# Performance work log

Measured on AMD Instinct MI355X. Metric: run time of the kernel, lower is better.

The kernel has to match this reference:

```python
import jax, jax.numpy as jnp
import numpy as np
import math

K = 8
MOMENTUM = 0.999


def _gelu(x):
    c = math.sqrt(2.0 / math.pi)
    return 0.5 * x * (1.0 + jnp.tanh(c * (x + 0.044715 * x ** 3)))


def _normalize(v, eps=1e-12):
    n = jnp.linalg.norm(v, axis=-1, keepdims=True)
    return v / jnp.maximum(n, eps)


def setup_inputs() -> dict:
    key = jax.random.key(0)
    k1, k2 = jax.random.split(key)
    B, T, D = 4, 4096, 2048
    x = jax.random.normal(k1, (B, T, D), dtype=jnp.float32)
    prototypes = _normalize(jax.random.normal(k2, (K, D), dtype=jnp.float32))
    log_tau = jnp.asarray(math.log(2.0), dtype=jnp.float32)
    log_blend = jnp.asarray(math.log(0.3 / 0.7), dtype=jnp.float32)
    return {"x": x, "prototypes": prototypes, "log_tau": log_tau, "log_blend": log_blend}


def reference(x, prototypes, log_tau, log_blend):
    tau = jnp.exp(log_tau)
    alpha = jax.nn.sigmoid(log_blend)
    B, T, D = x.shape
    x_flat = jax.lax.stop_gradient(x.reshape(-1, D))  # [N, D], detached

    P_norm = _normalize(prototypes)                  # [K, D]
    xn = _normalize(x_flat, eps=1e-8)                # [N, D]

    sims = jnp.clip(xn @ P_norm.T, -1.0, 1.0)        # [N, K]
    assignments = jnp.argmax(sims, axis=-1)          # [N]

    # masked per-cluster mean via segment-sum (vectorized over K)
    sums = jax.ops.segment_sum(x_flat, assignments, num_segments=K)       # [K, D]
    counts = jax.ops.segment_sum(jnp.ones((x_flat.shape[0],), x.dtype),
                                 assignments, num_segments=K)             # [K]
    has = (counts > 0)[:, None]
    centroids = jnp.where(has, sums / jnp.maximum(counts, 1.0)[:, None], prototypes)
    new_P = _normalize(centroids)

    P2 = MOMENTUM * prototypes + (1.0 - MOMENTUM) * new_P
    P2n = _normalize(P2, eps=1e-8)

    sims2 = jnp.clip(xn @ P2n.T, -1.0, 1.0)          # [N, K]
    dists = jnp.clip(1.0 - jnp.max(sims2, axis=-1), 0.0, 2.0)
    novelty = (1.0 - jnp.exp(-tau * dists)).reshape(B, T)

    scale = jnp.clip(1.0 - alpha + alpha * novelty[..., None], 0.1, 10.0)
    return _gelu(x * scale)
```

## Files before the change

kernel.cpp:

```cpp
#include <hip/hip_runtime.h>

#define DDIM  2048
#define KC    8
#define NCH   32
#define TPB_A 16
#define TPB_C 16

typedef float nfloat4 __attribute__((ext_vector_type(4)));
typedef unsigned short ushortv8 __attribute__((ext_vector_type(8)));
typedef unsigned short ushortv4 __attribute__((ext_vector_type(4)));

__device__ __forceinline__ void nt_store4(const float4& v, float* p){
  nfloat4 nv; nv.x = v.x; nv.y = v.y; nv.z = v.z; nv.w = v.w;
  __builtin_nontemporal_store(nv, (nfloat4*)p);
}

__device__ __forceinline__ unsigned short f2bf(float f){
  unsigned u = __float_as_uint(f);
  u += 0x7fffu + ((u >> 16) & 1u);
  return (unsigned short)(u >> 16);
}
__device__ __forceinline__ float bf2f(unsigned short h){
  return __uint_as_float(((unsigned)h) << 16);
}
__device__ __forceinline__ float bflo(unsigned u){ return __uint_as_float(u << 16); }
__device__ __forceinline__ float bfhi(unsigned u){ return __uint_as_float(u & 0xffff0000u); }

__device__ __forceinline__ float wave_sum(float v){
  #pragma unroll
  for (int off = 32; off > 0; off >>= 1)
    v += __shfl_xor(v, off, 64);
  return v;
}

__device__ __forceinline__ float butterfly8(float v[8], int t){
  {
    const bool h = (t & 1);
    #pragma unroll
    for (int j = 0; j < 4; ++j){
      float s    = h ? v[j]   : v[j+4];
      float keep = h ? v[j+4] : v[j];
      v[j] = keep + __shfl_xor(s, 1, 64);
    }
  }
  {
    const bool h = (t & 2);
    #pragma unroll
    for (int j = 0; j < 2; ++j){
      float s    = h ? v[j]   : v[j+2];
      float keep = h ? v[j+2] : v[j];
      v[j] = keep + __shfl_xor(s, 2, 64);
    }
  }
  {
    const bool h = (t & 4);
    float s    = h ? v[0] : v[1];
    float keep = h ? v[1] : v[0];
    v[0] = keep + __shfl_xor(s, 4, 64);
  }
  v[0] += __shfl_xor(v[0], 8, 64);
  v[0] += __shfl_xor(v[0], 16, 64);
  v[0] += __shfl_xor(v[0], 32, 64);
  return v[0];
}

__device__ __forceinline__ float gelu_tanh(float v){
  const float c = 0.7978845608028654f;
  float tt = c * v * (1.0f + 0.044715f * v * v);
  float e  = __expf(2.0f * tt);
  float th = 1.0f - 2.0f / (e + 1.0f);
  return 0.5f * v * (1.0f + th);
}

__global__ __launch_bounds__(256)
void k_pre(const float* __restrict__ proto, unsigned short* __restrict__ pbf)
{
  const int k = blockIdx.x, t = threadIdx.x;
  const int wave = t >> 6, lane = t & 63;
  __shared__ float sred[4];
  const int d0 = 4*t, d1 = 1024 + 4*t;
  float4 a = *(const float4*)(proto + k*DDIM + d0);
  float4 b = *(const float4*)(proto + k*DDIM + d1);
  float ss = a.x*a.x + a.y*a.y + a.z*a.z + a.w*a.w
           + b.x*b.x + b.y*b.y + b.z*b.z + b.w*b.w;
  ss = wave_sum(ss);
  if (lane == 0) sred[wave] = ss;
  __syncthreads();
  ss = sred[0] + sred[1] + sred[2] + sred[3];
  const float inv = 1.0f / fmaxf(sqrtf(ss), 1e-12f);
  ushortv4 o0, o1;
  o0[0]=f2bf(a.x*inv); o0[1]=f2bf(a.y*inv); o0[2]=f2bf(a.z*inv); o0[3]=f2bf(a.w*inv);
  o1[0]=f2bf(b.x*inv); o1[1]=f2bf(b.y*inv); o1[2]=f2bf(b.z*inv); o1[3]=f2bf(b.w*inv);
  *(ushortv4*)(pbf + k*DDIM + d0) = o0;
  *(ushortv4*)(pbf + k*DDIM + d1) = o1;
}

__global__ __launch_bounds__(256, 4)
void k_assign(const float* __restrict__ x, const unsigned short* __restrict__ pbf,
              unsigned short* __restrict__ part, float* __restrict__ pcnts, int ntok)
{
  __shared__ unsigned short Pl[KC*DDIM];
  __shared__ int asg[TPB_A];

  const int t = threadIdx.x;
  const int wave = t >> 6, lane = t & 63;

  #pragma unroll
  for (int j = 0; j < 8; ++j){
    const int e = (j*256 + t)*8;
    *(ushortv8*)(Pl + e) = *(const ushortv8*)(pbf + e);
  }
  __syncthreads();

  const int tok_base = blockIdx.x * TPB_A;

  {
    const int tl0 = wave*4;
    float4 X[8], N[8];
    int tok = tok_base + tl0;
    if (tok < ntok){
      #pragma unroll
      for (int j = 0; j < 8; ++j)
        X[j] = *(const float4*)(x + (size_t)tok*DDIM + j*256 + 4*lane);
    }
    #pragma unroll
    for (int i = 0; i < 4; ++i){
      const int tok_i = tok_base + tl0 + i;
      const bool ldn = (i < 3) && (tok_i + 1 < ntok);
      if (ldn){
        #pragma unroll
        for (int j = 0; j < 8; ++j)
          N[j] = *(const float4*)(x + (size_t)(tok_i+1)*DDIM + j*256 + 4*lane);
      }
      if (tok_i < ntok){
        float v[KC];
        #pragma unroll
        for (int k = 0; k < KC; ++k){
          float s = 0.f;
          #pragma unroll
          for (int j = 0; j < 8; ++j){
            uint2 u = *(const uint2*)((const unsigned*)Pl + k*1024 + j*128 + 2*lane);
            s += X[j].x*bflo(u.x) + X[j].y*bfhi(u.x)
               + X[j].z*bflo(u.y) + X[j].w*bfhi(u.y);
          }
          v[k] = s;
        }
        float bv = butterfly8(v, lane);
        int   bi = ((lane&1)<<2) | (lane&2) | ((lane>>2)&1);
        #pragma unroll
        for (int off = 1; off < 8; off <<= 1){
          float ov = __shfl_xor(bv, off, 64);
          int   oi = __shfl_xor(bi, off, 64);
          if (ov > bv || (ov == bv && oi < bi)){ bv = ov; bi = oi; }
        }
        if (lane == 0) asg[tl0 + i] = bi;
      }
      if (ldn){
        #pragma unroll
        for (int j = 0; j < 8; ++j) X[j] = N[j];
      }
    }
  }
  __syncthreads();

  const int d0 = 4*t, d1 = 1024 + 4*t;
  float4 acc0[KC], acc1[KC];
  float cnt[KC];
  #pragma unroll
  for (int k = 0; k < KC; ++k){
    acc0[k] = make_float4(0.f,0.f,0.f,0.f);
    acc1[k] = make_float4(0.f,0.f,0.f,0.f);
    cnt[k] = 0.f;
  }
  #pragma unroll
  for (int i = 0; i < TPB_A; ++i){
    const int tok = tok_base + i;
    if (tok < ntok){
      const int a = __builtin_amdgcn_readfirstlane(asg[i]);
      float4 xa = *(const float4*)(x + (size_t)tok*DDIM + d0);
      float4 xb = *(const float4*)(x + (size_t)tok*DDIM + d1);
      #pragma unroll
      for (int k = 0; k < KC; ++k){
        if (a == k){
          acc0[k].x += xa.x; acc0[k].y += xa.y; acc0[k].z += xa.z; acc0[k].w += xa.w;
          acc1[k].x += xb.x; acc1[k].y += xb.y; acc1[k].z += xb.z; acc1[k].w += xb.w;
          cnt[k] += 1.f;
        }
      }
    }
  }
  unsigned short* dst = part + (size_t)blockIdx.x * (KC*DDIM);
  #pragma unroll
  for (int k = 0; k < KC; ++k){
    ushortv4 o0, o1;
    o0[0]=f2bf(acc0[k].x); o0[1]=f2bf(acc0[k].y); o0[2]=f2bf(acc0[k].z); o0[3]=f2bf(acc0[k].w);
    o1[0]=f2bf(acc1[k].x); o1[1]=f2bf(acc1[k].y); o1[2]=f2bf(acc1[k].z); o1[3]=f2bf(acc1[k].w);
    *(ushortv4*)(dst + k*DDIM + d0) = o0;
    *(ushortv4*)(dst + k*DDIM + d1) = o1;
  }
  if (t == 0){
    #pragma unroll
    for (int k = 0; k < KC; ++k) pcnts[blockIdx.x*KC + k] = cnt[k];
  }
}

__global__ __launch_bounds__(256)
void k_reduce1(const unsigned short* __restrict__ part, const float* __restrict__ pcnts,
               float* __restrict__ stage2, float* __restrict__ cnt2, int nbA, int cs)
{
  const int ch = blockIdx.x >> 3;
  const int g  = blockIdx.x & 7;
  const int t  = threadIdx.x;
  const int col = g*2048 + t*8;
  const int b0 = ch*cs;

  float acc[8] = {0.f,0.f,0.f,0.f,0.f,0.f,0.f,0.f};
  for (int i = 0; i < cs; ++i){
    const int b = b0 + i;
    if (b < nbA){
      ushortv8 v = *(const ushortv8*)(part + (size_t)b*(KC*DDIM) + col);
      #pragma unroll
      for (int j = 0; j < 8; ++j) acc[j] += bf2f(v[j]);
    }
  }
  float4 o0 = make_float4(acc[0],acc[1],acc[2],acc[3]);
  float4 o1 = make_float4(acc[4],acc[5],acc[6],acc[7]);
  *(float4*)(stage2 + (size_t)ch*(KC*DDIM) + col)     = o0;
  *(float4*)(stage2 + (size_t)ch*(KC*DDIM) + col + 4) = o1;

  if (g == 0 && t < KC){
    float c = 0.f;
    for (int i = 0; i < cs; ++i){
      const int b = b0 + i;
      if (b < nbA) c += pcnts[b*KC + t];
    }
    cnt2[ch*KC + t] = c;
  }
}

__global__ __launch_bounds__(256)
void k_mid(const float* __restrict__ stage2, const float* __restrict__ cnt2,
           const float* __restrict__ proto, unsigned short* __restrict__ p2nbf)
{
  const int k = blockIdx.x, t = threadIdx.x;
  const int wave = t >> 6, lane = t & 63;
  __shared__ float s1[4], s2[4];
  const int d0 = 4*t, d1 = 1024 + 4*t;

  float4 a = make_float4(0.f,0.f,0.f,0.f), b = make_float4(0.f,0.f,0.f,0.f);
  #pragma unroll
  for (int ch = 0; ch < NCH; ++ch){
    const float* p = stage2 + (size_t)ch*(KC*DDIM) + k*DDIM;
    float4 u = *(const float4*)(p + d0);
    float4 w = *(const float4*)(p + d1);
    a.x += u.x; a.y += u.y; a.z += u.z; a.w += u.w;
    b.x += w.x; b.y += w.y; b.z += w.z; b.w += w.w;
  }
  float c = 0.f;
  #pragma unroll
  for (int ch = 0; ch < NCH; ++ch) c += cnt2[ch*KC + k];

  float4 pr0 = *(const float4*)(proto + k*DDIM + d0);
  float4 pr1 = *(const float4*)(proto + k*DDIM + d1);

  float4 c0, c1;
  if (c > 0.f){
    const float inv = 1.0f / fmaxf(c, 1.0f);
    c0.x=a.x*inv; c0.y=a.y*inv; c0.z=a.z*inv; c0.w=a.w*inv;
    c1.x=b.x*inv; c1.y=b.y*inv; c1.z=b.z*inv; c1.w=b.w*inv;
  } else { c0 = pr0; c1 = pr1; }

  float ss = c0.x*c0.x + c0.y*c0.y + c0.z*c0.z + c0.w*c0.w
           + c1.x*c1.x + c1.y*c1.y + c1.z*c1.z + c1.w*c1.w;
  ss = wave_sum(ss);
  if (lane == 0) s1[wave] = ss;
  __syncthreads();
  ss = s1[0] + s1[1] + s1[2] + s1[3];
  const float invc = 1.0f / fmaxf(sqrtf(ss), 1e-12f);

  const float m = 0.999f, om = 1.0f - 0.999f;
  float4 p20, p21;
  p20.x = m*pr0.x + om*c0.x*invc; p20.y = m*pr0.y + om*c0.y*invc;
  p20.z = m*pr0.z + om*c0.z*invc; p20.w = m*pr0.w + om*c0.w*invc;
  p21.x = m*pr1.x + om*c1.x*invc; p21.y = m*pr1.y + om*c1.y*invc;
  p21.z = m*pr1.z + om*c1.z*invc; p21.w = m*pr1.w + om*c1.w*invc;

  float ss2 = p20.x*p20.x + p20.y*p20.y + p20.z*p20.z + p20.w*p20.w
            + p21.x*p21.x + p21.y*p21.y + p21.z*p21.z + p21.w*p21.w;
  ss2 = wave_sum(ss2);
  if (lane == 0) s2[wave] = ss2;
  __syncthreads();
  ss2 = s2[0] + s2[1] + s2[2] + s2[3];
  const float inv2 = 1.0f / fmaxf(sqrtf(ss2), 1e-8f);

  ushortv4 o0, o1;
  o0[0]=f2bf(p20.x*inv2); o0[1]=f2bf(p20.y*inv2); o0[2]=f2bf(p20.z*inv2); o0[3]=f2bf(p20.w*inv2);
  o1[0]=f2bf(p21.x*inv2); o1[1]=f2bf(p21.y*inv2); o1[2]=f2bf(p21.z*inv2); o1[3]=f2bf(p21.w*inv2);
  *(ushortv4*)(p2nbf + k*DDIM + d0) = o0;
  *(ushortv4*)(p2nbf + k*DDIM + d1) = o1;
}

__global__ __launch_bounds__(256, 4)
void k_final(const float* __restrict__ x, const unsigned short* __restrict__ p2nbf,
             const float* __restrict__ plt, const float* __restrict__ plb,
             float* __restrict__ out, int ntok)
{
  __shared__ unsigned short Pl[KC*DDIM];
  const int t = threadIdx.x;
  const int wave = t >> 6, lane = t & 63;

  #pragma unroll
  for (int j = 0; j < 8; ++j){
    const int e = (j*256 + t)*8;
    *(ushortv8*)(Pl + e) = *(const ushortv8*)(p2nbf + e);
  }
  __syncthreads();

  const float tau   = __expf(plt[0]);
  const float alpha = 1.0f / (1.0f + __expf(-plb[0]));

  const int tl0 = wave*4;
  const int tok_base = blockIdx.x * TPB_C;
  float4 X[8], N[8];
  {
    const int tok = tok_base + tl0;
    if (tok < ntok){
      #pragma unroll
      for (int j = 0; j < 8; ++j)
        X[j] = *(const float4*)(x + (size_t)tok*DDIM + j*256 + 4*lane);
    }
  }
  #pragma unroll
  for (int i = 0; i < 4; ++i){
    const int tok_i = tok_base + tl0 + i;
    const bool ldn = (i < 3) && (tok_i + 1 < ntok);
    if (ldn){
      #pragma unroll
      for (int j = 0; j < 8; ++j)
        N[j] = *(const float4*)(x + (size_t)(tok_i+1)*DDIM + j*256 + 4*lane);
    }
    if (tok_i < ntok){
      float ss = 0.f;
      #pragma unroll
      for (int j = 0; j < 8; ++j)
        ss += X[j].x*X[j].x + X[j].y*X[j].y + X[j].z*X[j].z + X[j].w*X[j].w;
      ss = wave_sum(ss);

      float v[KC];
      #pragma unroll
      for (int k = 0; k < KC; ++k){
        float s = 0.f;
        #pragma unroll
        for (int j = 0; j < 8; ++j){
          uint2 u = *(const uint2*)((const unsigned*)Pl + k*1024 + j*128 + 2*lane);
          s += X[j].x*bflo(u.x) + X[j].y*bfhi(u.x)
             + X[j].z*bflo(u.y) + X[j].w*bfhi(u.y);
        }
        v[k] = s;
      }
      float mx = butterfly8(v, lane);
      mx = fmaxf(mx, __shfl_xor(mx, 1, 64));
      mx = fmaxf(mx, __shfl_xor(mx, 2, 64));
      mx = fmaxf(mx, __shfl_xor(mx, 4, 64));

      const float inv  = 1.0f / fmaxf(sqrtf(ss), 1e-8f);
      const float s    = fminf(fmaxf(mx * inv, -1.0f), 1.0f);
      const float dist = fminf(fmaxf(1.0f - s, 0.0f), 2.0f);
      const float nov  = 1.0f - __expf(-tau * dist);
      float sc = 1.0f - alpha + alpha * nov;
      sc = fminf(fmaxf(sc, 0.1f), 10.0f);

      float* o = out + (size_t)tok_i*DDIM;
      #pragma unroll
      for (int j = 0; j < 8; ++j){
        float4 g;
        g.x = gelu_tanh(X[j].x*sc); g.y = gelu_tanh(X[j].y*sc);
        g.z = gelu_tanh(X[j].z*sc); g.w = gelu_tanh(X[j].w*sc);
        nt_store4(g, o + j*256 + 4*lane);
      }
    }
    if (ldn){
      #pragma unroll
      for (int j = 0; j < 8; ++j) X[j] = N[j];
    }
  }
}

extern "C" void kernel_launch(void* const* d_in, const int* in_sizes, int n_in,
                              void* d_out, int out_size, void* d_ws, size_t ws_size,
                              hipStream_t stream)
{
  const float* x         = (const float*)d_in[0];
  const float* proto     = (const float*)d_in[1];
  const float* log_tau   = (const float*)d_in[2];
  const float* log_blend = (const float*)d_in[3];
  float* out = (float*)d_out;
  float* ws  = (float*)d_ws;

  const int ntok = in_sizes[0] / DDIM;

  unsigned short* pbf    = (unsigned short*)(ws);
  unsigned short* p2nbf  = (unsigned short*)(ws + 8192);
  float*          pcnts  = ws + 16384;
  float*          cnt2   = ws + 24576;
  float*          stage2 = ws + 24832;
  unsigned short* part   = (unsigned short*)(ws + 549120);

  const int nbA = (ntok + TPB_A - 1) / TPB_A;
  const int nbC = (ntok + TPB_C - 1) / TPB_C;
  const int cs  = (nbA + NCH - 1) / NCH;

  k_pre    <<<KC,     256, 0, stream>>>(proto, pbf);
  k_assign <<<nbA,    256, 0, stream>>>(x, pbf, part, pcnts, ntok);
  k_reduce1<<<NCH*8,  256, 0, stream>>>(part, pcnts, stage2, cnt2, nbA, cs);
  k_mid    <<<KC,     256, 0, stream>>>(stage2, cnt2, proto, p2nbf);
  k_final  <<<nbC,    256, 0, stream>>>(x, p2nbf, log_tau, log_blend, out, ntok);
}
```

Baseline: 306.4 us.

## Fuse prototype normalization into assign, double tokens per block, single-pass reduce

Removes the separate prototype-normalization kernel by having every assign block normalize the prototypes into shared memory. Tokens per block are doubled in both assign and final, which halves the number of partial-sum slabs. The two-stage chunked reduction is replaced by one reduce kernel that sums across all blocks for each (cluster, column slice), and partial-sum traffic now uses nontemporal stores and loads. In exchange, each assign block repeats the prototype norm work, and there is less block-level parallelism. The counts reduction assumes nbA is at most 512.

```diff
diff --git a/kernel.cpp b/kernel.cpp
--- a/kernel.cpp
+++ b/kernel.cpp
@@ -2,9 +2,8 @@
 
 #define DDIM  2048
 #define KC    8
-#define NCH   32
-#define TPB_A 16
-#define TPB_C 16
+#define TPB_A 32
+#define TPB_C 32
 
 typedef float nfloat4 __attribute__((ext_vector_type(4)));
 typedef unsigned short ushortv8 __attribute__((ext_vector_type(8)));
@@ -13,6 +12,12 @@
 __device__ __forceinline__ void nt_store4(const float4& v, float* p){
   nfloat4 nv; nv.x = v.x; nv.y = v.y; nv.z = v.z; nv.w = v.w;
   __builtin_nontemporal_store(nv, (nfloat4*)p);
+}
+__device__ __forceinline__ void nt_store_us4(const ushortv4& v, unsigned short* p){
+  __builtin_nontemporal_store(v, (ushortv4*)p);
+}
+__device__ __forceinline__ ushortv8 nt_load_us8(const unsigned short* p){
+  return __builtin_nontemporal_load((const ushortv8*)p);
 }
 
 __device__ __forceinline__ unsigned short f2bf(float f){
@@ -72,61 +77,68 @@
   return 0.5f * v * (1.0f + th);
 }
 
-__global__ __launch_bounds__(256)
-void k_pre(const float* __restrict__ proto, unsigned short* __restrict__ pbf)
-{
-  const int k = blockIdx.x, t = threadIdx.x;
-  const int wave = t >> 6, lane = t & 63;
-  __shared__ float sred[4];
-  const int d0 = 4*t, d1 = 1024 + 4*t;
-  float4 a = *(const float4*)(proto + k*DDIM + d0);
-  float4 b = *(const float4*)(proto + k*DDIM + d1);
-  float ss = a.x*a.x + a.y*a.y + a.z*a.z + a.w*a.w
-           + b.x*b.x + b.y*b.y + b.z*b.z + b.w*b.w;
-  ss = wave_sum(ss);
-  if (lane == 0) sred[wave] = ss;
-  __syncthreads();
-  ss = sred[0] + sred[1] + sred[2] + sred[3];
-  const float inv = 1.0f / fmaxf(sqrtf(ss), 1e-12f);
-  ushortv4 o0, o1;
-  o0[0]=f2bf(a.x*inv); o0[1]=f2bf(a.y*inv); o0[2]=f2bf(a.z*inv); o0[3]=f2bf(a.w*inv);
-  o1[0]=f2bf(b.x*inv); o1[1]=f2bf(b.y*inv); o1[2]=f2bf(b.z*inv); o1[3]=f2bf(b.w*inv);
-  *(ushortv4*)(pbf + k*DDIM + d0) = o0;
-  *(ushortv4*)(pbf + k*DDIM + d1) = o1;
-}
-
 __global__ __launch_bounds__(256, 4)
-void k_assign(const float* __restrict__ x, const unsigned short* __restrict__ pbf,
+void k_assign(const float* __restrict__ x, const float* __restrict__ proto,
               unsigned short* __restrict__ part, float* __restrict__ pcnts, int ntok)
 {
   __shared__ unsigned short Pl[KC*DDIM];
-  __shared__ int asg[TPB_A];
+  __shared__ float rednorm[4*KC];
+  __shared__ float sInv[KC];
+  __shared__ int   asg[TPB_A];
 
   const int t = threadIdx.x;
   const int wave = t >> 6, lane = t & 63;
-
-  #pragma unroll
-  for (int j = 0; j < 8; ++j){
-    const int e = (j*256 + t)*8;
-    *(ushortv8*)(Pl + e) = *(const ushortv8*)(pbf + e);
+  const int d0 = 4*t, d1 = 1024 + 4*t;
+
+  {
+    float4 Q0[KC], Q1[KC];
+    #pragma unroll
+    for (int k = 0; k < KC; ++k){
+      Q0[k] = *(const float4*)(proto + k*DDIM + d0);
+      Q1[k] = *(const float4*)(proto + k*DDIM + d1);
+    }
+    #pragma unroll
+    for (int k = 0; k < KC; ++k){
+      float ss = Q0[k].x*Q0[k].x + Q0[k].y*Q0[k].y + Q0[k].z*Q0[k].z + Q0[k].w*Q0[k].w
+               + Q1[k].x*Q1[k].x + Q1[k].y*Q1[k].y + Q1[k].z*Q1[k].z + Q1[k].w*Q1[k].w;
+      ss = wave_sum(ss);
+      if (lane == 0) rednorm[wave*KC + k] = ss;
+    }
+    __syncthreads();
+    if (t < KC){
+      float ss = rednorm[t] + rednorm[KC+t] + rednorm[2*KC+t] + rednorm[3*KC+t];
+      sInv[t] = 1.0f / fmaxf(sqrtf(ss), 1e-12f);
+    }
+    __syncthreads();
+    #pragma unroll
+    for (int k = 0; k < KC; ++k){
+      const float inv = sInv[k];
+      ushortv4 o0, o1;
+      o0[0]=f2bf(Q0[k].x*inv); o0[1]=f2bf(Q0[k].y*inv); o0[2]=f2bf(Q0[k].z*inv); o0[3]=f2bf(Q0[k].w*inv);
+      o1[0]=f2bf(Q1[k].x*inv); o1[1]=f2bf(Q1[k].y*inv); o1[2]=f2bf(Q1[k].z*inv); o1[3]=f2bf(Q1[k].w*inv);
+      *(ushortv4*)(Pl + k*DDIM + d0) = o0;
+      *(ushortv4*)(Pl + k*DDIM + d1) = o1;
+    }
   }
   __syncthreads();
 
   const int tok_base = blockIdx.x * TPB_A;
 
   {
-    const int tl0 = wave*4;
+    const int tl0 = wave*8;
     float4 X[8], N[8];
-    int tok = tok_base + tl0;
-    if (tok < ntok){
-      #pragma unroll
-      for (int j = 0; j < 8; ++j)
-        X[j] = *(const float4*)(x + (size_t)tok*DDIM + j*256 + 4*lane);
-    }
-    #pragma unroll
-    for (int i = 0; i < 4; ++i){
+    {
+      const int tok = tok_base + tl0;
+      if (tok < ntok){
+        #pragma unroll
+        for (int j = 0; j < 8; ++j)
+          X[j] = *(const float4*)(x + (size_t)tok*DDIM + j*256 + 4*lane);
+      }
+    }
+    #pragma unroll
+    for (int i = 0; i < 8; ++i){
       const int tok_i = tok_base + tl0 + i;
-      const bool ldn = (i < 3) && (tok_i + 1 < ntok);
+      const bool ldn = (i < 7) && (tok_i + 1 < ntok);
       if (ldn){
         #pragma unroll
         for (int j = 0; j < 8; ++j)
@@ -163,7 +175,6 @@
   }
   __syncthreads();
 
-  const int d0 = 4*t, d1 = 1024 + 4*t;
   float4 acc0[KC], acc1[KC];
   float cnt[KC];
   #pragma unroll
@@ -195,8 +206,8 @@
     ushortv4 o0, o1;
     o0[0]=f2bf(acc0[k].x); o0[1]=f2bf(acc0[k].y); o0[2]=f2bf(acc0[k].z); o0[3]=f2bf(acc0[k].w);
     o1[0]=f2bf(acc1[k].x); o1[1]=f2bf(acc1[k].y); o1[2]=f2bf(acc1[k].z); o1[3]=f2bf(acc1[k].w);
-    *(ushortv4*)(dst + k*DDIM + d0) = o0;
-    *(ushortv4*)(dst + k*DDIM + d1) = o1;
+    nt_store_us4(o0, dst + k*DDIM + d0);
+    nt_store_us4(o1, dst + k*DDIM + d1);
   }
   if (t == 0){
     #pragma unroll
@@ -205,41 +216,50 @@
 }
 
 __global__ __launch_bounds__(256)
-void k_reduce1(const unsigned short* __restrict__ part, const float* __restrict__ pcnts,
-               float* __restrict__ stage2, float* __restrict__ cnt2, int nbA, int cs)
+void k_reduce(const unsigned short* __restrict__ part, const float* __restrict__ pcnts,
+              float* __restrict__ csum, float* __restrict__ ccnt, int nbA)
 {
-  const int ch = blockIdx.x >> 3;
-  const int g  = blockIdx.x & 7;
-  const int t  = threadIdx.x;
-  const int col = g*2048 + t*8;
-  const int b0 = ch*cs;
-
-  float acc[8] = {0.f,0.f,0.f,0.f,0.f,0.f,0.f,0.f};
-  for (int i = 0; i < cs; ++i){
-    const int b = b0 + i;
-    if (b < nbA){
-      ushortv8 v = *(const ushortv8*)(part + (size_t)b*(KC*DDIM) + col);
-      #pragma unroll
-      for (int j = 0; j < 8; ++j) acc[j] += bf2f(v[j]);
-    }
-  }
-  float4 o0 = make_float4(acc[0],acc[1],acc[2],acc[3]);
-  float4 o1 = make_float4(acc[4],acc[5],acc[6],acc[7]);
-  *(float4*)(stage2 + (size_t)ch*(KC*DDIM) + col)     = o0;
-  *(float4*)(stage2 + (size_t)ch*(KC*DDIM) + col + 4) = o1;
-
-  if (g == 0 && t < KC){
-    float c = 0.f;
-    for (int i = 0; i < cs; ++i){
-      const int b = b0 + i;
-      if (b < nbA) c += pcnts[b*KC + t];
-    }
-    cnt2[ch*KC + t] = c;
-  }
+  const int k = blockIdx.x >> 4;
+  const int s = blockIdx.x & 15;
+  const int t = threadIdx.x;
+  const int slot = t & 15;
+  const int grp  = t >> 4;
+
+  __shared__ float cmb[16][16][8];
+  __shared__ float credn[4];
+
+  const size_t ebase = (size_t)k*DDIM + s*128 + slot*8;
+  float a[8] = {0.f,0.f,0.f,0.f,0.f,0.f,0.f,0.f};
+  for (int b = grp; b < nbA; b += 16){
+    ushortv8 v = nt_load_us8(part + (size_t)b*(KC*DDIM) + ebase);
+    #pragma unroll
+    for (int j = 0; j < 8; ++j) a[j] += bf2f(v[j]);
+  }
+  #pragma unroll
+  for (int j = 0; j < 8; ++j) cmb[grp][slot][j] = a[j];
+
+  float c = 0.f;
+  if (s == 0){
+    if (t < nbA)        c += pcnts[t*KC + k];
+    if (t + 256 < nbA)  c += pcnts[(t+256)*KC + k];
+    c = wave_sum(c);
+    if ((t & 63) == 0) credn[t >> 6] = c;
+  }
+  __syncthreads();
+
+  if (t < 128){
+    const int slot2 = t >> 3, j = t & 7;
+    float sum = 0.f;
+    #pragma unroll
+    for (int g = 0; g < 16; ++g) sum += cmb[g][slot2][j];
+    csum[(size_t)k*DDIM + s*128 + slot2*8 + j] = sum;
+  }
+  if (s == 0 && t == 0)
+    ccnt[k] = credn[0] + credn[1] + credn[2] + credn[3];
 }
 
 __global__ __launch_bounds__(256)
-void k_mid(const float* __restrict__ stage2, const float* __restrict__ cnt2,
+void k_mid(const float* __restrict__ csum, const float* __restrict__ ccnt,
            const float* __restrict__ proto, unsigned short* __restrict__ p2nbf)
 {
   const int k = blockIdx.x, t = threadIdx.x;
@@ -247,18 +267,9 @@
   __shared__ float s1[4], s2[4];
   const int d0 = 4*t, d1 = 1024 + 4*t;
 
-  float4 a = make_float4(0.f,0.f,0.f,0.f), b = make_float4(0.f,0.f,0.f,0.f);
-  #pragma unroll
-  for (int ch = 0; ch < NCH; ++ch){
-    const float* p = stage2 + (size_t)ch*(KC*DDIM) + k*DDIM;
-    float4 u = *(const float4*)(p + d0);
-    float4 w = *(const float4*)(p + d1);
-    a.x += u.x; a.y += u.y; a.z += u.z; a.w += u.w;
-    b.x += w.x; b.y += w.y; b.z += w.z; b.w += w.w;
-  }
-  float c = 0.f;
-  #pragma unroll
-  for (int ch = 0; ch < NCH; ++ch) c += cnt2[ch*KC + k];
+  float4 a = *(const float4*)(csum + k*DDIM + d0);
+  float4 b = *(const float4*)(csum + k*DDIM + d1);
+  const float c = ccnt[k];
 
   float4 pr0 = *(const float4*)(proto + k*DDIM + d0);
   float4 pr1 = *(const float4*)(proto + k*DDIM + d1);
@@ -319,7 +330,7 @@
   const float tau   = __expf(plt[0]);
   const float alpha = 1.0f / (1.0f + __expf(-plb[0]));
 
-  const int tl0 = wave*4;
+  const int tl0 = wave*8;
   const int tok_base = blockIdx.x * TPB_C;
   float4 X[8], N[8];
   {
@@ -331,9 +342,9 @@
     }
   }
   #pragma unroll
-  for (int i = 0; i < 4; ++i){
+  for (int i = 0; i < 8; ++i){
     const int tok_i = tok_base + tl0 + i;
-    const bool ldn = (i < 3) && (tok_i + 1 < ntok);
+    const bool ldn = (i < 7) && (tok_i + 1 < ntok);
     if (ldn){
       #pragma unroll
       for (int j = 0; j < 8; ++j)
@@ -399,20 +410,17 @@
 
   const int ntok = in_sizes[0] / DDIM;
 
-  unsigned short* pbf    = (unsigned short*)(ws);
-  unsigned short* p2nbf  = (unsigned short*)(ws + 8192);
-  float*          pcnts  = ws + 16384;
-  float*          cnt2   = ws + 24576;
-  float*          stage2 = ws + 24832;
-  unsigned short* part   = (unsigned short*)(ws + 549120);
+  unsigned short* p2nbf = (unsigned short*)(ws);
+  float*          pcnts = ws + 8192;
+  float*          csum  = ws + 12288;
+  float*          ccnt  = ws + 28672;
+  unsigned short* part  = (unsigned short*)(ws + 28688);
 
   const int nbA = (ntok + TPB_A - 1) / TPB_A;
   const int nbC = (ntok + TPB_C - 1) / TPB_C;
-  const int cs  = (nbA + NCH - 1) / NCH;
-
-  k_pre    <<<KC,     256, 0, stream>>>(proto, pbf);
-  k_assign <<<nbA,    256, 0, stream>>>(x, pbf, part, pcnts, ntok);
-  k_reduce1<<<NCH*8,  256, 0, stream>>>(part, pcnts, stage2, cnt2, nbA, cs);
-  k_mid    <<<KC,     256, 0, stream>>>(stage2, cnt2, proto, p2nbf);
-  k_final  <<<nbC,    256, 0, stream>>>(x, p2nbf, log_tau, log_blend, out, ntok);
-}
+
+  k_assign<<<nbA, 256, 0, stream>>>(x, proto, part, pcnts, ntok);
+  k_reduce<<<128, 256, 0, stream>>>(part, pcnts, csum, ccnt, nbA);
+  k_mid   <<<KC,  256, 0, stream>>>(csum, ccnt, proto, p2nbf);
+  k_final <<<nbC, 256, 0, stream>>>(x, p2nbf, log_tau, log_blend, out, ntok);
+}
```

After: 333.4 us. +8.8%, slower.

## Replace two-level chunked partial reduction with single-pass per-cluster column reduce

Applied to the files above, without the earlier changes.

The two-stage reduction (chunked partials into a stage2 buffer, then summed again in k_mid) is replaced by one k_reduce kernel. Each block owns a 64-element column strip of one cluster, strides over all partial blocks with 32 thread groups, and combines them in shared memory, so the stage2 buffer and k_mid's 32-way re-summation go away. The partial writes and reads now use nontemporal stores and loads to avoid polluting the cache. The readfirstlane on the assignment index is also dropped, which could make the branch non-uniform to the compiler and add scalar-to-vector overhead in k_assign.

```diff
diff --git a/kernel.cpp b/kernel.cpp
--- a/kernel.cpp
+++ b/kernel.cpp
@@ -2,7 +2,6 @@
 
 #define DDIM  2048
 #define KC    8
-#define NCH   32
 #define TPB_A 16
 #define TPB_C 16
 
@@ -13,6 +12,12 @@
 __device__ __forceinline__ void nt_store4(const float4& v, float* p){
   nfloat4 nv; nv.x = v.x; nv.y = v.y; nv.z = v.z; nv.w = v.w;
   __builtin_nontemporal_store(nv, (nfloat4*)p);
+}
+__device__ __forceinline__ void nt_store_us4(const ushortv4& v, unsigned short* p){
+  __builtin_nontemporal_store(v, (ushortv4*)p);
+}
+__device__ __forceinline__ ushortv8 nt_load_us8(const unsigned short* p){
+  return __builtin_nontemporal_load((const ushortv8*)p);
 }
 
 __device__ __forceinline__ unsigned short f2bf(float f){
@@ -176,7 +181,7 @@
   for (int i = 0; i < TPB_A; ++i){
     const int tok = tok_base + i;
     if (tok < ntok){
-      const int a = __builtin_amdgcn_readfirstlane(asg[i]);
+      const int a = asg[i];
       float4 xa = *(const float4*)(x + (size_t)tok*DDIM + d0);
       float4 xb = *(const float4*)(x + (size_t)tok*DDIM + d1);
       #pragma unroll
@@ -195,8 +200,8 @@
     ushortv4 o0, o1;
     o0[0]=f2bf(acc0[k].x); o0[1]=f2bf(acc0[k].y); o0[2]=f2bf(acc0[k].z); o0[3]=f2bf(acc0[k].w);
     o1[0]=f2bf(acc1[k].x); o1[1]=f2bf(acc1[k].y); o1[2]=f2bf(acc1[k].z); o1[3]=f2bf(acc1[k].w);
-    *(ushortv4*)(dst + k*DDIM + d0) = o0;
-    *(ushortv4*)(dst + k*DDIM + d1) = o1;
+    nt_store_us4(o0, dst + k*DDIM + d0);
+    nt_store_us4(o1, dst + k*DDIM + d1);
   }
   if (t == 0){
     #pragma unroll
@@ -205,41 +210,49 @@
 }
 
 __global__ __launch_bounds__(256)
-void k_reduce1(const unsigned short* __restrict__ part, const float* __restrict__ pcnts,
-               float* __restrict__ stage2, float* __restrict__ cnt2, int nbA, int cs)
-{
-  const int ch = blockIdx.x >> 3;
-  const int g  = blockIdx.x & 7;
-  const int t  = threadIdx.x;
-  const int col = g*2048 + t*8;
-  const int b0 = ch*cs;
-
-  float acc[8] = {0.f,0.f,0.f,0.f,0.f,0.f,0.f,0.f};
-  for (int i = 0; i < cs; ++i){
-    const int b = b0 + i;
-    if (b < nbA){
-      ushortv8 v = *(const ushortv8*)(part + (size_t)b*(KC*DDIM) + col);
-      #pragma unroll
-      for (int j = 0; j < 8; ++j) acc[j] += bf2f(v[j]);
-    }
-  }
-  float4 o0 = make_float4(acc[0],acc[1],acc[2],acc[3]);
-  float4 o1 = make_float4(acc[4],acc[5],acc[6],acc[7]);
-  *(float4*)(stage2 + (size_t)ch*(KC*DDIM) + col)     = o0;
-  *(float4*)(stage2 + (size_t)ch*(KC*DDIM) + col + 4) = o1;
-
-  if (g == 0 && t < KC){
-    float c = 0.f;
-    for (int i = 0; i < cs; ++i){
-      const int b = b0 + i;
-      if (b < nbA) c += pcnts[b*KC + t];
-    }
-    cnt2[ch*KC + t] = c;
-  }
+void k_reduce(const unsigned short* __restrict__ part, const float* __restrict__ pcnts,
+              float* __restrict__ csum, float* __restrict__ ccnt, int nbA)
+{
+  const int k = blockIdx.x >> 5;
+  const int s = blockIdx.x & 31;
+  const int t = threadIdx.x;
+  const int slot = t & 7;
+  const int grp  = t >> 3;
+
+  __shared__ float cmb[32][8][8];
+  __shared__ float credn[4];
+
+  const size_t ebase = (size_t)k*DDIM + s*64 + slot*8;
+  float a[8] = {0.f,0.f,0.f,0.f,0.f,0.f,0.f,0.f};
+  for (int b = grp; b < nbA; b += 32){
+    ushortv8 v = nt_load_us8(part + (size_t)b*(KC*DDIM) + ebase);
+    #pragma unroll
+    for (int j = 0; j < 8; ++j) a[j] += bf2f(v[j]);
+  }
+  #pragma unroll
+  for (int j = 0; j < 8; ++j) cmb[grp][slot][j] = a[j];
+
+  float c = 0.f;
+  if (s == 0){
+    for (int b = t; b < nbA; b += 256) c += pcnts[b*KC + k];
+    c = wave_sum(c);
+    if ((t & 63) == 0) credn[t >> 6] = c;
+  }
+  __syncthreads();
+
+  if (t < 64){
+    const int slot2 = t >> 3, j = t & 7;
+    float sum = 0.f;
+    #pragma unroll
+    for (int g = 0; g < 32; ++g) sum += cmb[g][slot2][j];
+    csum[(size_t)k*DDIM + s*64 + slot2*8 + j] = sum;
+  }
+  if (s == 0 && t == 0)
+    ccnt[k] = credn[0] + credn[1] + credn[2] + credn[3];
 }
 
 __global__ __launch_bounds__(256)
-void k_mid(const float* __restrict__ stage2, const float* __restrict__ cnt2,
+void k_mid(const float* __restrict__ csum, const float* __restrict__ ccnt,
            const float* __restrict__ proto, unsigned short* __restrict__ p2nbf)
 {
   const int k = blockIdx.x, t = threadIdx.x;
@@ -247,18 +260,9 @@
   __shared__ float s1[4], s2[4];
   const int d0 = 4*t, d1 = 1024 + 4*t;
 
-  float4 a = make_float4(0.f,0.f,0.f,0.f), b = make_float4(0.f,0.f,0.f,0.f);
-  #pragma unroll
-  for (int ch = 0; ch < NCH; ++ch){
-    const float* p = stage2 + (size_t)ch*(KC*DDIM) + k*DDIM;
-    float4 u = *(const float4*)(p + d0);
-    float4 w = *(const float4*)(p + d1);
-    a.x += u.x; a.y += u.y; a.z += u.z; a.w += u.w;
-    b.x += w.x; b.y += w.y; b.z += w.z; b.w += w.w;
-  }
-  float c = 0.f;
-  #pragma unroll
-  for (int ch = 0; ch < NCH; ++ch) c += cnt2[ch*KC + k];
+  float4 a = *(const float4*)(csum + k*DDIM + d0);
+  float4 b = *(const float4*)(csum + k*DDIM + d1);
+  const float c = ccnt[k];
 
   float4 pr0 = *(const float4*)(proto + k*DDIM + d0);
   float4 pr1 = *(const float4*)(proto + k*DDIM + d1);
@@ -399,20 +403,19 @@
 
   const int ntok = in_sizes[0] / DDIM;
 
-  unsigned short* pbf    = (unsigned short*)(ws);
-  unsigned short* p2nbf  = (unsigned short*)(ws + 8192);
-  float*          pcnts  = ws + 16384;
-  float*          cnt2   = ws + 24576;
-  float*          stage2 = ws + 24832;
-  unsigned short* part   = (unsigned short*)(ws + 549120);
+  unsigned short* pbf   = (unsigned short*)(ws);
+  unsigned short* p2nbf = (unsigned short*)(ws + 8192);
+  float*          pcnts = ws + 16384;
+  float*          csum  = ws + 24576;
+  float*          ccnt  = ws + 40960;
+  unsigned short* part  = (unsigned short*)(ws + 40976);
 
   const int nbA = (ntok + TPB_A - 1) / TPB_A;
   const int nbC = (ntok + TPB_C - 1) / TPB_C;
-  const int cs  = (nbA + NCH - 1) / NCH;
-
-  k_pre    <<<KC,     256, 0, stream>>>(proto, pbf);
-  k_assign <<<nbA,    256, 0, stream>>>(x, pbf, part, pcnts, ntok);
-  k_reduce1<<<NCH*8,  256, 0, stream>>>(part, pcnts, stage2, cnt2, nbA, cs);
-  k_mid    <<<KC,     256, 0, stream>>>(stage2, cnt2, proto, p2nbf);
-  k_final  <<<nbC,    256, 0, stream>>>(x, p2nbf, log_tau, log_blend, out, ntok);
-}
+
+  k_pre   <<<KC,  256, 0, stream>>>(proto, pbf);
+  k_assign<<<nbA, 256, 0, stream>>>(x, pbf, part, pcnts, ntok);
+  k_reduce<<<256, 256, 0, stream>>>(part, pcnts, csum, ccnt, nbA);
+  k_mid   <<<KC,  256, 0, stream>>>(csum, ccnt, proto, p2nbf);
+  k_final <<<nbC, 256, 0, stream>>>(x, p2nbf, log_tau, log_blend, out, ntok);
+}
```

After: 309.2 us. Within noise of the previous version (+0.9%).
